# Performance work log

Measured on AMD Instinct MI355X. Metric: run time of the kernel, lower is better.

The kernel has to match this reference:

```python
import jax, jax.numpy as jnp
import numpy as np

B, G, C = 32, 50, 80
IMG = 640
STRIDES = (8, 16, 32)
CENTER_RADIUS = 2.5


def _make_grids():
    xs, ys, ss = [], [], []
    for s in STRIDES:
        n = IMG // s
        yv, xv = np.meshgrid(np.arange(n, dtype=np.float32), np.arange(n, dtype=np.float32), indexing='ij')
        xs.append(xv.reshape(-1)); ys.append(yv.reshape(-1))
        ss.append(np.full(n * n, s, dtype=np.float32))
    return np.concatenate(xs), np.concatenate(ys), np.concatenate(ss)


def setup_inputs():
    xg, yg, sg = _make_grids()
    A = xg.shape[0]  # 8400
    ks = jax.random.split(jax.random.key(0), 5)
    # decoded box predictions near grid centers (cxcywh, pixel units)
    ctr = jnp.stack([jnp.asarray((xg + 0.5) * sg), jnp.asarray((yg + 0.5) * sg)], -1)[None] \
        + jax.random.normal(ks[0], (B, A, 2)) * 8.0
    wh = jnp.exp(jax.random.normal(ks[1], (B, A, 2)) * 0.5) * jnp.asarray(sg)[None, :, None] * 4.0
    pred_output = jnp.concatenate([ctr, wh, jax.random.normal(ks[2], (B, A, 1 + C))], -1)  # [B,A,85]
    obj_preds = jax.random.normal(ks[3], (B, A, 1))
    cls_preds = jax.random.normal(ks[4], (B, A, C))
    # labels [B,G,5] = (class, cx, cy, w, h); first num_gt rows valid, rest zero
    rng = np.random.RandomState(0)
    lab = np.zeros((B, G, 5), np.float32)
    for b in range(B):
        ng = rng.randint(5, G)
        lab[b, :ng, 0] = rng.randint(0, C, ng)
        lab[b, :ng, 1:3] = rng.uniform(40.0, IMG - 40.0, (ng, 2))
        lab[b, :ng, 3:5] = rng.uniform(20.0, 160.0, (ng, 2))
    return {"pred_output": pred_output, "obj_preds": obj_preds, "cls_preds": cls_preds,
            "labels": jnp.asarray(lab), "x_shifts": jnp.asarray(xg),
            "y_shifts": jnp.asarray(yg), "strides": jnp.asarray(sg)}


def _pairwise_iou_cxcywh(a, b):
    # a [G,4], b [A,4] -> [G,A]
    tl = jnp.maximum(a[:, None, :2] - a[:, None, 2:] * 0.5, b[None, :, :2] - b[None, :, 2:] * 0.5)
    br = jnp.minimum(a[:, None, :2] + a[:, None, 2:] * 0.5, b[None, :, :2] + b[None, :, 2:] * 0.5)
    area_a = a[:, 2] * a[:, 3]
    area_b = b[:, 2] * b[:, 3]
    en = jnp.all(tl < br, -1).astype(a.dtype)
    area_i = jnp.prod(br - tl, -1) * en
    return area_i / (area_a[:, None] + area_b[None, :] - area_i + 1e-16)


def _assign_one(gt, gt_valid, boxes, cls_logit, obj_logit, xg, yg, sg):
    # SimOTA assignment for a single image, fully vectorized over [G,A].
    # gt [G,5], gt_valid [G], boxes [A,4], cls_logit [A,C], obj_logit [A,1]
    num_gt = gt.shape[0]
    gt_cls = gt[:, 0].astype(jnp.int32)
    gb = gt[:, 1:5]
    xc = (xg + 0.5) * sg
    yc = (yg + 0.5) * sg
    d_box = jnp.stack([
        xc[None, :] - (gb[:, 0:1] - gb[:, 2:3] * 0.5),
        (gb[:, 0:1] + gb[:, 2:3] * 0.5) - xc[None, :],
        yc[None, :] - (gb[:, 1:2] - gb[:, 3:4] * 0.5),
        (gb[:, 1:2] + gb[:, 3:4] * 0.5) - yc[None, :]], -1)
    in_boxes = (jnp.min(d_box, -1) > 0) & gt_valid[:, None]
    d_ctr = jnp.stack([
        xc[None, :] - (gb[:, 0:1] - CENTER_RADIUS * sg[None, :]),
        (gb[:, 0:1] + CENTER_RADIUS * sg[None, :]) - xc[None, :],
        yc[None, :] - (gb[:, 1:2] - CENTER_RADIUS * sg[None, :]),
        (gb[:, 1:2] + CENTER_RADIUS * sg[None, :]) - yc[None, :]], -1)
    in_ctr = (jnp.min(d_ctr, -1) > 0) & gt_valid[:, None]
    fg0 = jnp.any(in_boxes | in_ctr, 0)           # [A] candidate anchors (fg_mask)
    and_ctr = in_boxes & in_ctr                    # [G,A]
    ious = _pairwise_iou_cxcywh(gb, boxes) * fg0[None, :].astype(boxes.dtype) * gt_valid[:, None].astype(boxes.dtype)
    # pairwise BCE(sqrt(sig(cls)*sig(obj)), one_hot) summed over classes, without [G,A,C]
    logq = 0.5 * (jax.nn.log_sigmoid(cls_logit) + jax.nn.log_sigmoid(obj_logit))  # [A,C]
    q = jnp.clip(jnp.exp(logq), 1e-7, 1.0 - 1e-7)
    s_neg = jnp.sum(jnp.log1p(-q), -1)             # [A] sum_c log(1-q_c)
    q_gt = q[:, gt_cls].T                          # [G,A]
    cls_cost = -jnp.log(q_gt) + jnp.log1p(-q_gt) - s_neg[None, :]
    invalid = (~fg0)[None, :] | (~gt_valid)[:, None]
    cost = cls_cost - 3.0 * jnp.log(ious + 1e-8) + 1e5 * (~and_ctr) + 1e9 * invalid
    # dynamic-k: sum of top-10 ious per gt, truncated, min 1
    dyn_k = jnp.maximum(jnp.sum(jax.lax.top_k(ious, 10)[0], -1).astype(jnp.int32), 1)  # [G]
    ranks = jnp.argsort(jnp.argsort(cost, 1), 1)   # rank of each anchor in ascending cost
    matching = (ranks < dyn_k[:, None]) & gt_valid[:, None]
    # resolve anchors claimed by >1 gt: keep min-cost gt
    best_gt = jnp.argmin(cost, 0)                  # [A]
    onehot_best = jnp.arange(num_gt)[:, None] == best_gt[None, :]
    matching = jnp.where(jnp.sum(matching, 0)[None, :] > 1, onehot_best, matching)
    fg = jnp.any(matching, 0)                      # [A] final fg mask
    matched = jnp.argmax(matching, 0)              # [A] matched gt index
    pred_iou = jnp.sum(matching * ious, 0)         # [A]
    cls_t = jax.nn.one_hot(gt_cls[matched], cls_logit.shape[-1], dtype=boxes.dtype) \
        * (pred_iou * fg.astype(boxes.dtype))[:, None]
    return cls_t, fg, matched


def _forward(pred_output, obj_preds, cls_preds, labels, x_shifts, y_shifts, strides):
    bbox = pred_output[:, :, :4]
    gt_valid = labels.sum(-1) > 0
    cls_t, fg, matched = jax.vmap(_assign_one, in_axes=(0, 0, 0, 0, 0, None, None, None))(
        labels, gt_valid, bbox, cls_preds, obj_preds, x_shifts, y_shifts, strides)
    cls_t = jax.lax.stop_gradient(cls_t)  # get_assignments is @torch.no_grad()
    reg_t = jnp.take_along_axis(labels[:, :, 1:5], matched[:, :, None], axis=1)  # [B,A,4]
    fg_f = fg.astype(pred_output.dtype)
    num_fg = jnp.maximum(jnp.sum(fg_f), 1.0)
    # IoU loss (cxcywh), loss = 1 - iou^2, only on fg anchors
    tl = jnp.maximum(bbox[..., :2] - bbox[..., 2:] * 0.5, reg_t[..., :2] - reg_t[..., 2:] * 0.5)
    br = jnp.minimum(bbox[..., :2] + bbox[..., 2:] * 0.5, reg_t[..., :2] + reg_t[..., 2:] * 0.5)
    en = jnp.all(tl < br, -1).astype(bbox.dtype)
    area_i = jnp.prod(br - tl, -1) * en
    area_u = bbox[..., 2] * bbox[..., 3] + reg_t[..., 2] * reg_t[..., 3] - area_i
    iou = area_i / (area_u + 1e-16)
    loss_iou = jnp.sum((1.0 - iou ** 2) * fg_f) / num_fg
    bce = lambda x, y: jax.nn.softplus(x) - x * y  # BCEWithLogits, reduction='none'
    loss_obj = jnp.sum(bce(obj_preds[..., 0], fg_f)) / num_fg
    loss_cls = jnp.sum(bce(cls_preds, cls_t) * fg_f[..., None]) / num_fg
    return 5.0 * loss_iou + loss_obj + loss_cls


def reference(pred_output, obj_preds, cls_preds, labels, x_shifts, y_shifts, strides):
    return _forward(pred_output, obj_preds, cls_preds, labels, x_shifts, y_shifts, strides)
```

## Files before the change

### kernel.cpp

```cpp
#include <hip/hip_runtime.h>
#include <cstdint>
#include <cstddef>

#define BB 32
#define GG 50
#define CC 80
#define AA 8400
#define PCH (5 + CC)
#define NLB ((BB * AA + 255) / 256)
#define FGBIT 63
#define SENTC 3.3e38f
#define SENTI 0x7fffffff

__device__ __forceinline__ float logsig_fast(float x) {
    float e = __expf(-fabsf(x));
    return fminf(x, 0.f) - __logf(1.f + e);
}
__device__ __forceinline__ float softplusf(float x) {
    return fmaxf(x, 0.f) + log1pf(expf(-fabsf(x)));
}

__device__ __forceinline__ float pair_iou(float px, float py, float pw, float ph,
                                          float gx, float gy, float gw, float gh) {
    float tlx = fmaxf(gx - gw * 0.5f, px - pw * 0.5f);
    float tly = fmaxf(gy - gh * 0.5f, py - ph * 0.5f);
    float brx = fminf(gx + gw * 0.5f, px + pw * 0.5f);
    float bry = fminf(gy + gh * 0.5f, py + ph * 0.5f);
    float en = (tlx < brx && tly < bry) ? 1.f : 0.f;
    float ai = (brx - tlx) * (bry - tly) * en;
    return ai / (gw * gh + pw * ph - ai + 1e-16f);
}
__device__ __forceinline__ float cost_val(float x , float lo ,
                                          float sn , float v ,
                                          bool ac, bool f0, bool valid) {
    float lq = 0.5f * (logsig_fast(x) + lo);
    float q = fminf(fmaxf(__expf(lq), 1e-7f), 1.f - 1e-7f);
    float cst = -__logf(q) + __logf(1.f - q) - sn;
    cst -= 3.0f * __logf(v + 1e-8f);
    cst += 100000.0f * (ac ? 0.f : 1.f);
    cst += 1000000000.0f * ((!f0 || !valid) ? 1.f : 0.f);
    return cst;
}

__global__ __launch_bounds__(256)
void k_precompute(const float* __restrict__ pred, const float* __restrict__ obj,
                  const float* __restrict__ cls,
                  float2* __restrict__ lsn, float* __restrict__ sps,
                  float4* __restrict__ pbox) {
    int t = blockIdx.x * blockDim.x + threadIdx.x;
    int i = t >> 2;
    int sub = t & 3;
    if (i >= BB * AA) return;
    float lo = logsig_fast(obj[i]);
    float K = __expf(0.5f * lo);
    const float4* c4 = (const float4*)(cls + (size_t)i * CC);
    float smax = 0.f, psp = 1.f, p1 = 1.f, p2 = 1.f;
#pragma unroll
    for (int j = 0; j < 5; j++) {
        float4 v = c4[sub + 4 * j];
        float xs4[4] = {v.x, v.y, v.z, v.w};
        float pg = 1.f;
#pragma unroll
        for (int u = 0; u < 4; u++) {
            float x = xs4[u];
            float th = __expf(-0.5f * fabsf(x));
            float t2 = th * th;
            smax += fmaxf(x, 0.f);
            psp *= (1.f + t2);
            float qq = K * (x < 0.f ? th : 1.f) * rsqrtf(1.f + t2);
            qq = fminf(fmaxf(qq, 1e-7f), 1.f - 1e-7f);
            pg *= (1.f - qq);
        }
        if (j < 2) p1 *= pg; else p2 *= pg;
    }
    float sp = smax + __logf(psp);
    float sn = __logf(p1) + __logf(p2);
    sp += __shfl_xor(sp, 1); sn += __shfl_xor(sn, 1);
    sp += __shfl_xor(sp, 2); sn += __shfl_xor(sn, 2);
    float pv = pred[(size_t)i * PCH + sub];
    ((float*)pbox)[(size_t)i * 4 + sub] = pv;
    if (sub == 0) {
        lsn[i] = make_float2(lo, sn);
        sps[i] = sp;
    }
}

__global__ void k_geom(const float* __restrict__ labels, const float* __restrict__ xs,
                       const float* __restrict__ ys, const float* __restrict__ ss,
                       const float4* __restrict__ pbox, const float2* __restrict__ lsn,
                       unsigned long long* __restrict__ amask,
                       int* __restrict__ clist, unsigned long long* __restrict__ camask,
                       float4* __restrict__ cpbox, float2* __restrict__ clsn,
                       int* __restrict__ ccnt) {
    int b = blockIdx.y;
    int a = blockIdx.x * blockDim.x + threadIdx.x;
    __shared__ float lab[GG * 5];
    __shared__ int lv[GG];
    for (int t = threadIdx.x; t < GG * 5; t += blockDim.x) lab[t] = labels[b * GG * 5 + t];
    __syncthreads();
    if (threadIdx.x < GG) {
        const float* r = lab + threadIdx.x * 5;
        lv[threadIdx.x] = ((r[0] + r[1] + r[2] + r[3] + r[4]) > 0.f) ? 1 : 0;
    }
    __syncthreads();
    if (a >= AA) return;
    float s = ss[a];
    float xc = (xs[a] + 0.5f) * s;
    float yc = (ys[a] + 0.5f) * s;
    unsigned long long m = 0;
    int any = 0;
    for (int g = 0; g < GG; g++) {
        if (!lv[g]) continue;
        const float* r = lab + g * 5;
        float gx = r[1], gy = r[2], gw = r[3], gh = r[4];
        float d1 = xc - (gx - gw * 0.5f);
        float d2 = (gx + gw * 0.5f) - xc;
        float d3 = yc - (gy - gh * 0.5f);
        float d4 = (gy + gh * 0.5f) - yc;
        bool ib = fminf(fminf(d1, d2), fminf(d3, d4)) > 0.f;
        float cr = 2.5f * s;
        float e1 = xc - (gx - cr);
        float e2 = (gx + cr) - xc;
        float e3 = yc - (gy - cr);
        float e4 = (gy + cr) - yc;
        bool ic = fminf(fminf(e1, e2), fminf(e3, e4)) > 0.f;
        if (ib || ic) any = 1;
        if (ib && ic) m |= 1ull << g;
    }
    if (any) m |= 1ull << FGBIT;
    amask[b * AA + a] = m;
    int lane = threadIdx.x & 63;
    unsigned long long act = __ballot(m != 0);
    if (act) {
        int leader = __ffsll(act) - 1;
        int base = 0;
        if (lane == leader) base = atomicAdd(&ccnt[b], __popcll(act));
        base = __shfl(base, leader);
        if (m != 0) {
            int off = __popcll(act & ((1ull << lane) - 1ull));
            int pos = b * AA + base + off;
            clist[pos] = a;
            camask[pos] = m;
            cpbox[pos] = pbox[b * AA + a];
            clsn[pos] = lsn[b * AA + a];
        }
    }
}

__global__ __launch_bounds__(256, 4)
void k_assign(const float4* __restrict__ pbox, const float2* __restrict__ lsn,
              const float* __restrict__ cls,
              const unsigned long long* __restrict__ amask,
              const float* __restrict__ labels,
              const int* __restrict__ clist, const unsigned long long* __restrict__ camask,
              const float4* __restrict__ cpbox, const float2* __restrict__ clsn,
              const int* __restrict__ ccnt,
              unsigned long long* __restrict__ mmask) {
    int w = blockIdx.x;
    int b = w / GG, g = w % GG;
    const float* r = labels + (size_t)w * 5;
    float gcls = r[0], gx = r[1], gy = r[2], gw = r[3], gh = r[4];
    if (!((gcls + gx + gy + gw + gh) > 0.f)) return;
    int gtc = (int)gcls;
    int tid = threadIdx.x;
    int lane = tid & 63;
    int wv = tid >> 6;
    int cnt = ccnt[b];

    float ivl[10];
    float cvl[10];
    int   cil[10];
#pragma unroll
    for (int t = 0; t < 10; t++) { ivl[t] = 0.f; cvl[t] = SENTC; cil[t] = SENTI; }
    int nlc = 0;

    for (int i0 = wv * 64 + lane; i0 < cnt; i0 += 256) {
        int pos = b * AA + i0;
        unsigned long long am = camask[pos];
        float4 pb = cpbox[pos];
        bool ac = (am >> g) & 1ull;
        nlc += ac ? 1 : 0;
        float v = pair_iou(pb.x, pb.y, pb.z, pb.w, gx, gy, gw, gh);
        if (v > ivl[9]) {
            float mv = v;
#pragma unroll
            for (int t = 0; t < 10; t++)
                if (mv > ivl[t]) { float tmp = ivl[t]; ivl[t] = mv; mv = tmp; }
        }
        if (ac) {
            int a = clist[pos];
            float2 ls = clsn[pos];
            float c = cost_val(cls[((size_t)b * AA + a) * CC + gtc], ls.x, ls.y, v,
                               true, true, true);
            int id = a;
            if (c < cvl[9] || (c == cvl[9] && id < cil[9])) {
#pragma unroll
                for (int t = 0; t < 10; t++) {
                    bool sw = (c < cvl[t]) || (c == cvl[t] && id < cil[t]);
                    if (sw) {
                        float tf = cvl[t]; cvl[t] = c; c = tf;
                        int ti = cil[t]; cil[t] = id; id = ti;
                    }
                }
            }
        }
    }

    __shared__ float IV[4][10];
    __shared__ float CV[4][10];
    __shared__ int CI[4][10];
    __shared__ int NAC[4];
    __shared__ int s_k, s_n0;
    __shared__ int sel[10];

    {
        int s = nlc;
#pragma unroll
        for (int off = 1; off < 64; off <<= 1) s += __shfl_xor(s, off);
        if (lane == 0) NAC[wv] = s;
    }

    for (int rr = 0; rr < 10; rr++) {
        float bv = ivl[0];
        int bl = lane;
#pragma unroll
        for (int off = 1; off < 64; off <<= 1) {
            float ov = __shfl_xor(bv, off);
            int ol = __shfl_xor(bl, off);
            if (ov > bv || (ov == bv && ol < bl)) { bv = ov; bl = ol; }
        }
        if (lane == 0) IV[wv][rr] = bv;
        if (lane == bl) {
#pragma unroll
            for (int t = 0; t < 9; t++) ivl[t] = ivl[t + 1];
            ivl[9] = 0.f;
        }
    }

    for (int rr = 0; rr < 10; rr++) {
        float bc = cvl[0];
        int bi = cil[0];
        int bl = lane;
#pragma unroll
        for (int off = 1; off < 64; off <<= 1) {
            float oc = __shfl_xor(bc, off);
            int oi = __shfl_xor(bi, off);
            int ol = __shfl_xor(bl, off);
            bool tk = (oc < bc) || (oc == bc && (oi < bi || (oi == bi && ol < bl)));
            if (tk) { bc = oc; bi = oi; bl = ol; }
        }
        if (lane == 0) { CV[wv][rr] = bc; CI[wv][rr] = bi; }
        if (lane == bl) {
#pragma unroll
            for (int t = 0; t < 9; t++) { cvl[t] = cvl[t + 1]; cil[t] = cil[t + 1]; }
            cvl[9] = SENTC; cil[9] = SENTI;
        }
    }
    __syncthreads();

    if (tid == 0) {
        int h[4] = {0, 0, 0, 0};
        float ssum = 0.f;
        for (int j = 0; j < 10; j++) {
            float bv = -1.f; int bc = 0;
#pragma unroll
            for (int c2 = 0; c2 < 4; c2++)
                if (h[c2] < 10 && IV[c2][h[c2]] > bv) { bv = IV[c2][h[c2]]; bc = c2; }
            ssum += bv;
            h[bc]++;
        }
        int k = (int)ssum;
        if (k < 1) k = 1;
        s_k = k;
        s_n0 = NAC[0] + NAC[1] + NAC[2] + NAC[3];
    }
    __syncthreads();
    int k = s_k;

    if (s_n0 < k) {
#pragma unroll
        for (int t = 0; t < 10; t++) { cvl[t] = SENTC; cil[t] = SENTI; }
        const int chunk = AA / 4;
        int abase = wv * chunk, aend = abase + chunk;
        for (int a0 = abase; a0 < aend; a0 += 64) {
            int a = a0 + lane;
            bool inr = a < aend;
            int ia = b * AA + (inr ? a : (aend - 1));
            unsigned long long am = amask[ia];
            bool f0 = inr && ((am >> FGBIT) & 1ull);
            bool ac = inr && ((am >> g) & 1ull);
            float v = 0.f;
            if (f0) {
                float4 pb = pbox[ia];
                v = pair_iou(pb.x, pb.y, pb.z, pb.w, gx, gy, gw, gh);
            }
            float c = SENTC; int id = SENTI;
            if (inr) {
                float x = cls[(size_t)ia * CC + gtc];
                float2 ls = lsn[ia];
                c = cost_val(x, ls.x, ls.y, v, ac, f0, true);
                id = a;
            }
            if (c < cvl[9] || (c == cvl[9] && id < cil[9])) {
#pragma unroll
                for (int t = 0; t < 10; t++) {
                    bool sw = (c < cvl[t]) || (c == cvl[t] && id < cil[t]);
                    if (sw) {
                        float tf = cvl[t]; cvl[t] = c; c = tf;
                        int ti = cil[t]; cil[t] = id; id = ti;
                    }
                }
            }
        }
        for (int rr = 0; rr < 10; rr++) {
            float bc = cvl[0];
            int bi = cil[0];
            int bl = lane;
#pragma unroll
            for (int off = 1; off < 64; off <<= 1) {
                float oc = __shfl_xor(bc, off);
                int oi = __shfl_xor(bi, off);
                int ol = __shfl_xor(bl, off);
                bool tk = (oc < bc) || (oc == bc && (oi < bi || (oi == bi && ol < bl)));
                if (tk) { bc = oc; bi = oi; bl = ol; }
            }
            if (lane == 0) { CV[wv][rr] = bc; CI[wv][rr] = bi; }
            if (lane == bl) {
#pragma unroll
                for (int t = 0; t < 9; t++) { cvl[t] = cvl[t + 1]; cil[t] = cil[t + 1]; }
                cvl[9] = SENTC; cil[9] = SENTI;
            }
        }
        __syncthreads();
    }

    if (tid == 0) {
        int h[4] = {0, 0, 0, 0};
        for (int j = 0; j < k; j++) {
            float bv = SENTC; int bix = SENTI; int bc = 0;
#pragma unroll
            for (int c2 = 0; c2 < 4; c2++) {
                if (h[c2] < 10) {
                    float av = CV[c2][h[c2]]; int ax = CI[c2][h[c2]];
                    if (av < bv || (av == bv && ax < bix)) { bv = av; bix = ax; bc = c2; }
                }
            }
            sel[j] = bix;
            h[bc]++;
        }
    }
    __syncthreads();
    if (tid < k) {
        atomicOr(&mmask[(size_t)b * AA + sel[tid]], 1ull << g);
    }
}

__global__ void k_loss(const float4* __restrict__ pbox, const float* __restrict__ obj,
                       const float* __restrict__ cls, const float* __restrict__ labels,
                       const float2* __restrict__ lsn,
                       const unsigned long long* __restrict__ amask,
                       const unsigned long long* __restrict__ mmask,
                       const float* __restrict__ sps, float* __restrict__ partial) {
    int i = blockIdx.x * blockDim.x + threadIdx.x;
    float li = 0.f, lo = 0.f, lc = 0.f, nf = 0.f;
    if (i < BB * AA) {
        int b = i / AA, a = i % AA;
        unsigned long long m = mmask[i];
        int cnt = __popcll(m);
        bool fg = (m != 0);
        int mg = 0;
        float4 pb = pbox[i];
        unsigned long long am = amask[i];
        bool f0 = (am >> FGBIT) & 1ull;
        if (cnt > 1) {
            float2 ls = lsn[i];
            float bv = 3.4e38f;
            for (int g = 0; g < GG; g++) {
                const float* r = labels + (size_t)(b * GG + g) * 5;
                float gcls = r[0], gx = r[1], gy = r[2], gw = r[3], gh = r[4];
                bool valid = (gcls + gx + gy + gw + gh) > 0.f;
                int gtc = (int)gcls;
                float raw = pair_iou(pb.x, pb.y, pb.z, pb.w, gx, gy, gw, gh);
                float v = raw * (f0 ? 1.f : 0.f) * (valid ? 1.f : 0.f);
                float x = cls[(size_t)i * CC + gtc];
                bool ac = (am >> g) & 1ull;
                float cst = cost_val(x, ls.x, ls.y, v, ac, f0, valid);
                if (cst < bv) { bv = cst; mg = g; }
            }
        } else if (cnt == 1) {
            mg = __ffsll((unsigned long long)m) - 1;
        }
        float o = obj[i];
        lo = softplusf(o) - (fg ? o : 0.f);
        if (fg) {
            const float* r = labels + (size_t)(b * GG + mg) * 5;
            float gcls = r[0], gx = r[1], gy = r[2], gw = r[3], gh = r[4];
            bool valid = (gcls + gx + gy + gw + gh) > 0.f;
            int gtc = (int)gcls;
            float piou = pair_iou(pb.x, pb.y, pb.z, pb.w, gx, gy, gw, gh)
                         * (f0 ? 1.f : 0.f) * (valid ? 1.f : 0.f);
            float tlx = fmaxf(pb.x - pb.z * 0.5f, gx - gw * 0.5f);
            float tly = fmaxf(pb.y - pb.w * 0.5f, gy - gh * 0.5f);
            float brx = fminf(pb.x + pb.z * 0.5f, gx + gw * 0.5f);
            float bry = fminf(pb.y + pb.w * 0.5f, gy + gh * 0.5f);
            float en = (tlx < brx && tly < bry) ? 1.f : 0.f;
            float ai = (brx - tlx) * (bry - tly) * en;
            float u = pb.z * pb.w + gw * gh - ai;
            float v2 = ai / (u + 1e-16f);
            li = 1.f - v2 * v2;
            lc = sps[i] - cls[(size_t)i * CC + gtc] * piou;
            nf = 1.f;
        }
    }
    for (int off = 32; off; off >>= 1) {
        li += __shfl_down(li, off);
        lo += __shfl_down(lo, off);
        lc += __shfl_down(lc, off);
        nf += __shfl_down(nf, off);
    }
    __shared__ float red[4][4];
    int wid = threadIdx.x >> 6;
    if ((threadIdx.x & 63) == 0) {
        red[wid][0] = li; red[wid][1] = lo; red[wid][2] = lc; red[wid][3] = nf;
    }
    __syncthreads();
    if (threadIdx.x == 0) {
        float s0 = 0.f, s1 = 0.f, s2 = 0.f, s3 = 0.f;
#pragma unroll
        for (int t = 0; t < 4; t++) {
            s0 += red[t][0]; s1 += red[t][1]; s2 += red[t][2]; s3 += red[t][3];
        }
        float4* pb = (float4*)partial;
        pb[blockIdx.x] = make_float4(s0, s1, s2, s3);
    }
}

__global__ void k_final(const float* __restrict__ partial, float* __restrict__ out) {
    int tid = threadIdx.x;
    float s0 = 0.f, s1 = 0.f, s2 = 0.f, s3 = 0.f;
    const float4* pb = (const float4*)partial;
    for (int i = tid; i < NLB; i += 256) {
        float4 v = pb[i];
        s0 += v.x; s1 += v.y; s2 += v.z; s3 += v.w;
    }
    for (int off = 32; off; off >>= 1) {
        s0 += __shfl_down(s0, off);
        s1 += __shfl_down(s1, off);
        s2 += __shfl_down(s2, off);
        s3 += __shfl_down(s3, off);
    }
    __shared__ float red[4][4];
    int wid = tid >> 6;
    if ((tid & 63) == 0) {
        red[wid][0] = s0; red[wid][1] = s1; red[wid][2] = s2; red[wid][3] = s3;
    }
    __syncthreads();
    if (tid == 0) {
        float li = 0.f, lo = 0.f, lc = 0.f, nf = 0.f;
#pragma unroll
        for (int t = 0; t < 4; t++) {
            li += red[t][0]; lo += red[t][1]; lc += red[t][2]; nf += red[t][3];
        }
        nf = fmaxf(nf, 1.f);
        out[0] = (5.f * li + lo + lc) / nf;
    }
}

extern "C" void kernel_launch(void* const* d_in, const int* in_sizes, int n_in,
                              void* d_out, int out_size, void* d_ws, size_t ws_size,
                              hipStream_t stream) {
    const float* pred = (const float*)d_in[0];
    const float* obj  = (const float*)d_in[1];
    const float* cls  = (const float*)d_in[2];
    const float* lab  = (const float*)d_in[3];
    const float* xs   = (const float*)d_in[4];
    const float* ys   = (const float*)d_in[5];
    const float* ss   = (const float*)d_in[6];
    float* out = (float*)d_out;

    const size_t BA = (size_t)BB * AA;

    float4* pbox  = (float4*)d_ws;
    float4* cpbox = pbox + BA;
    float2* lsn   = (float2*)(cpbox + BA);
    float2* clsn  = lsn + BA;
    unsigned long long* amask  = (unsigned long long*)(clsn + BA);
    unsigned long long* camask = amask + BA;
    unsigned long long* mmask  = camask + BA;
    float* sps = (float*)(mmask + BA);
    float* partial = sps + BA;
    int* clist = (int*)(partial + (size_t)NLB * 4);
    int* ccnt  = clist + BA;

    hipMemsetAsync(mmask, 0, BA * sizeof(unsigned long long), stream);
    hipMemsetAsync(ccnt, 0, BB * sizeof(int), stream);

    dim3 blk(256);
    k_precompute<<<dim3((BB * AA * 4 + 255) / 256), blk, 0, stream>>>(pred, obj, cls,
                                                                      lsn, sps, pbox);
    k_geom<<<dim3((AA + 255) / 256, BB), blk, 0, stream>>>(lab, xs, ys, ss, pbox, lsn,
                                                           amask, clist, camask, cpbox,
                                                           clsn, ccnt);
    k_assign<<<dim3(BB * GG), blk, 0, stream>>>(pbox, lsn, cls, amask, lab,
                                                clist, camask, cpbox, clsn, ccnt, mmask);
    k_loss<<<dim3(NLB), blk, 0, stream>>>(pbox, obj, cls, lab, lsn, amask,
                                          mmask, sps, partial);
    k_final<<<1, blk, 0, stream>>>(partial, out);
}
```

Measured before the change: 154.1 us.

## Replace iterative wave top-k extraction with bitonic butterfly merge of padded lists

Per-lane top-k lists grow from 10 to 16 entries so that a bitonic merge network can combine them across the wavefront with xor shuffles. This replaces the previous approach of ten rounds of wave argmax reduction plus list shifting. It cuts serialized reduction rounds and shuffles, but adds more registers and larger per-lane insertion sorts, which may lower occupancy.

```diff
diff --git a/kernel.cpp b/kernel.cpp
--- a/kernel.cpp
+++ b/kernel.cpp
@@ -11,6 +11,7 @@
 #define FGBIT 63
 #define SENTC 3.3e38f
 #define SENTI 0x7fffffff
+#define LK 16
 
 __device__ __forceinline__ float logsig_fast(float x) {
     float e = __expf(-fabsf(x));
@@ -40,6 +41,57 @@
     cst += 100000.0f * (ac ? 0.f : 1.f);
     cst += 1000000000.0f * ((!f0 || !valid) ? 1.f : 0.f);
     return cst;
+}
+
+__device__ __forceinline__ void wave_merge_desc(float v[LK]) {
+#pragma unroll
+    for (int off = 1; off < 64; off <<= 1) {
+        float m[LK];
+#pragma unroll
+        for (int j = 0; j < LK; j++) m[j] = __shfl_xor(v[j], off);
+#pragma unroll
+        for (int j = 0; j < LK; j++) v[j] = fmaxf(v[j], m[LK - 1 - j]);
+#pragma unroll
+        for (int d = 8; d; d >>= 1) {
+#pragma unroll
+            for (int j = 0; j < LK; j++) {
+                if (!(j & d)) {
+                    float a = v[j], b = v[j + d];
+                    v[j] = fmaxf(a, b);
+                    v[j + d] = fminf(a, b);
+                }
+            }
+        }
+    }
+}
+
+__device__ __forceinline__ void wave_merge_asc(float c[LK], int ix[LK]) {
+#pragma unroll
+    for (int off = 1; off < 64; off <<= 1) {
+        float mc[LK];
+        int mi[LK];
+#pragma unroll
+        for (int j = 0; j < LK; j++) { mc[j] = __shfl_xor(c[j], off); mi[j] = __shfl_xor(ix[j], off); }
+#pragma unroll
+        for (int j = 0; j < LK; j++) {
+            float oc = mc[LK - 1 - j];
+            int oi = mi[LK - 1 - j];
+            bool tk = (oc < c[j]) || (oc == c[j] && oi < ix[j]);
+            if (tk) { c[j] = oc; ix[j] = oi; }
+        }
+#pragma unroll
+        for (int d = 8; d; d >>= 1) {
+#pragma unroll
+            for (int j = 0; j < LK; j++) {
+                if (!(j & d)) {
+                    float a = c[j], b = c[j + d];
+                    int ai = ix[j], bi = ix[j + d];
+                    bool sw = (b < a) || (b == a && bi < ai);
+                    if (sw) { c[j] = b; ix[j] = bi; c[j + d] = a; ix[j + d] = ai; }
+                }
+            }
+        }
+    }
 }
 
 __global__ __launch_bounds__(256)
@@ -167,11 +219,11 @@
     int wv = tid >> 6;
     int cnt = ccnt[b];
 
-    float ivl[10];
-    float cvl[10];
-    int   cil[10];
-#pragma unroll
-    for (int t = 0; t < 10; t++) { ivl[t] = 0.f; cvl[t] = SENTC; cil[t] = SENTI; }
+    float ivl[LK];
+    float cvl[LK];
+    int   cil[LK];
+#pragma unroll
+    for (int t = 0; t < LK; t++) { ivl[t] = 0.f; cvl[t] = SENTC; cil[t] = SENTI; }
     int nlc = 0;
 
     for (int i0 = wv * 64 + lane; i0 < cnt; i0 += 256) {
@@ -181,10 +233,10 @@
         bool ac = (am >> g) & 1ull;
         nlc += ac ? 1 : 0;
         float v = pair_iou(pb.x, pb.y, pb.z, pb.w, gx, gy, gw, gh);
-        if (v > ivl[9]) {
+        if (v > ivl[LK - 1]) {
             float mv = v;
 #pragma unroll
-            for (int t = 0; t < 10; t++)
+            for (int t = 0; t < LK; t++)
                 if (mv > ivl[t]) { float tmp = ivl[t]; ivl[t] = mv; mv = tmp; }
         }
         if (ac) {
@@ -193,9 +245,9 @@
             float c = cost_val(cls[((size_t)b * AA + a) * CC + gtc], ls.x, ls.y, v,
                                true, true, true);
             int id = a;
-            if (c < cvl[9] || (c == cvl[9] && id < cil[9])) {
-#pragma unroll
-                for (int t = 0; t < 10; t++) {
+            if (c < cvl[LK - 1] || (c == cvl[LK - 1] && id < cil[LK - 1])) {
+#pragma unroll
+                for (int t = 0; t < LK; t++) {
                     bool sw = (c < cvl[t]) || (c == cvl[t] && id < cil[t]);
                     if (sw) {
                         float tf = cvl[t]; cvl[t] = c; c = tf;
@@ -206,9 +258,9 @@
         }
     }
 
-    __shared__ float IV[4][10];
-    __shared__ float CV[4][10];
-    __shared__ int CI[4][10];
+    __shared__ float IV[4][LK];
+    __shared__ float CV[4][LK];
+    __shared__ int CI[4][LK];
     __shared__ int NAC[4];
     __shared__ int s_k, s_n0;
     __shared__ int sel[10];
@@ -220,41 +272,11 @@
         if (lane == 0) NAC[wv] = s;
     }
 
-    for (int rr = 0; rr < 10; rr++) {
-        float bv = ivl[0];
-        int bl = lane;
-#pragma unroll
-        for (int off = 1; off < 64; off <<= 1) {
-            float ov = __shfl_xor(bv, off);
-            int ol = __shfl_xor(bl, off);
-            if (ov > bv || (ov == bv && ol < bl)) { bv = ov; bl = ol; }
-        }
-        if (lane == 0) IV[wv][rr] = bv;
-        if (lane == bl) {
-#pragma unroll
-            for (int t = 0; t < 9; t++) ivl[t] = ivl[t + 1];
-            ivl[9] = 0.f;
-        }
-    }
-
-    for (int rr = 0; rr < 10; rr++) {
-        float bc = cvl[0];
-        int bi = cil[0];
-        int bl = lane;
-#pragma unroll
-        for (int off = 1; off < 64; off <<= 1) {
-            float oc = __shfl_xor(bc, off);
-            int oi = __shfl_xor(bi, off);
-            int ol = __shfl_xor(bl, off);
-            bool tk = (oc < bc) || (oc == bc && (oi < bi || (oi == bi && ol < bl)));
-            if (tk) { bc = oc; bi = oi; bl = ol; }
-        }
-        if (lane == 0) { CV[wv][rr] = bc; CI[wv][rr] = bi; }
-        if (lane == bl) {
-#pragma unroll
-            for (int t = 0; t < 9; t++) { cvl[t] = cvl[t + 1]; cil[t] = cil[t + 1]; }
-            cvl[9] = SENTC; cil[9] = SENTI;
-        }
+    wave_merge_desc(ivl);
+    wave_merge_asc(cvl, cil);
+    if (lane == 0) {
+#pragma unroll
+        for (int t = 0; t < LK; t++) { IV[wv][t] = ivl[t]; CV[wv][t] = cvl[t]; CI[wv][t] = cil[t]; }
     }
     __syncthreads();
 
@@ -265,7 +287,7 @@
             float bv = -1.f; int bc = 0;
 #pragma unroll
             for (int c2 = 0; c2 < 4; c2++)
-                if (h[c2] < 10 && IV[c2][h[c2]] > bv) { bv = IV[c2][h[c2]]; bc = c2; }
+                if (h[c2] < LK && IV[c2][h[c2]] > bv) { bv = IV[c2][h[c2]]; bc = c2; }
             ssum += bv;
             h[bc]++;
         }
@@ -279,7 +301,7 @@
 
     if (s_n0 < k) {
 #pragma unroll
-        for (int t = 0; t < 10; t++) { cvl[t] = SENTC; cil[t] = SENTI; }
+        for (int t = 0; t < LK; t++) { cvl[t] = SENTC; cil[t] = SENTI; }
         const int chunk = AA / 4;
         int abase = wv * chunk, aend = abase + chunk;
         for (int a0 = abase; a0 < aend; a0 += 64) {
@@ -301,9 +323,9 @@
                 c = cost_val(x, ls.x, ls.y, v, ac, f0, true);
                 id = a;
             }
-            if (c < cvl[9] || (c == cvl[9] && id < cil[9])) {
-#pragma unroll
-                for (int t = 0; t < 10; t++) {
+            if (c < cvl[LK - 1] || (c == cvl[LK - 1] && id < cil[LK - 1])) {
+#pragma unroll
+                for (int t = 0; t < LK; t++) {
                     bool sw = (c < cvl[t]) || (c == cvl[t] && id < cil[t]);
                     if (sw) {
                         float tf = cvl[t]; cvl[t] = c; c = tf;
@@ -312,24 +334,10 @@
                 }
             }
         }
-        for (int rr = 0; rr < 10; rr++) {
-            float bc = cvl[0];
-            int bi = cil[0];
-            int bl = lane;
-#pragma unroll
-            for (int off = 1; off < 64; off <<= 1) {
-                float oc = __shfl_xor(bc, off);
-                int oi = __shfl_xor(bi, off);
-                int ol = __shfl_xor(bl, off);
-                bool tk = (oc < bc) || (oc == bc && (oi < bi || (oi == bi && ol < bl)));
-                if (tk) { bc = oc; bi = oi; bl = ol; }
-            }
-            if (lane == 0) { CV[wv][rr] = bc; CI[wv][rr] = bi; }
-            if (lane == bl) {
-#pragma unroll
-                for (int t = 0; t < 9; t++) { cvl[t] = cvl[t + 1]; cil[t] = cil[t + 1]; }
-                cvl[9] = SENTC; cil[9] = SENTI;
-            }
+        wave_merge_asc(cvl, cil);
+        if (lane == 0) {
+#pragma unroll
+            for (int t = 0; t < LK; t++) { CV[wv][t] = cvl[t]; CI[wv][t] = cil[t]; }
         }
         __syncthreads();
     }
@@ -340,7 +348,7 @@
             float bv = SENTC; int bix = SENTI; int bc = 0;
 #pragma unroll
             for (int c2 = 0; c2 < 4; c2++) {
-                if (h[c2] < 10) {
+                if (h[c2] < LK) {
                     float av = CV[c2][h[c2]]; int ax = CI[c2][h[c2]];
                     if (av < bv || (av == bv && ax < bix)) { bv = av; bix = ax; bc = c2; }
                 }
```

New measurement: 165.6 us. +7.5%, slower.
